# Optimization experiments

Measured on AMD Instinct MI355X. Metric: run time of the kernel, lower is better.

Reference implementation:

```python
import jax, jax.numpy as jnp
import numpy as np

N_NODES = 50000
N_EDGES = 1000000
N_QUERY = 100000
NUM_FEATURES = 256
HIDDEN = 256
LABEL_DIM = 2


def glorot(key, shape):
    lim = float(np.sqrt(6.0 / (shape[0] + shape[1])))
    return jax.random.uniform(key, shape, jnp.float32, -lim, lim)


def setup_inputs() -> dict:
    key = jax.random.key(0)
    ks = jax.random.split(key, 8)
    x = jax.random.normal(ks[0], (N_NODES, NUM_FEATURES), jnp.float32)
    edge_index = jax.random.randint(ks[1], (2, N_EDGES), 0, N_NODES)
    query_edges = jax.random.randint(ks[2], (N_QUERY, 2), 0, N_NODES)
    edge_weight = jax.random.uniform(ks[3], (N_EDGES,), jnp.float32)
    W1 = glorot(ks[4], (NUM_FEATURES, HIDDEN))
    b1 = jnp.zeros((HIDDEN,), jnp.float32)
    W2 = glorot(ks[5], (HIDDEN, HIDDEN))
    b2 = jnp.zeros((HIDDEN,), jnp.float32)
    Wl = glorot(ks[6], (2 * HIDDEN, LABEL_DIM))
    bl = jnp.zeros((LABEL_DIM,), jnp.float32)
    return {"x": x, "edge_index": edge_index, "query_edges": query_edges,
            "edge_weight": edge_weight, "W1": W1, "b1": b1, "W2": W2,
            "b2": b2, "Wl": Wl, "bl": bl}


def digcn_conv(x, edge_index, edge_weight, W, b):
    # x: [N, F_in] -> h: [N, F_out]; propagate: out[dst] += w_e * h[src]
    h = x @ W
    src, dst = edge_index[0], edge_index[1]
    msg = h[src] * edge_weight[:, None]            # [E, F_out]
    agg = jax.ops.segment_sum(msg, dst, num_segments=x.shape[0])
    return agg + b


def reference(x, edge_index, query_edges, edge_weight, W1, b1, W2, b2, Wl, bl):
    h = jax.nn.relu(digcn_conv(x, edge_index, edge_weight, W1, b1))
    # dropout is identity at eval time
    h = digcn_conv(h, edge_index, edge_weight, W2, b2)
    q = jnp.concatenate((h[query_edges[:, 0]], h[query_edges[:, 1]]), axis=-1)
    logits = q @ Wl + bl
    return jax.nn.log_softmax(logits, axis=1)
```

## Files before the change

kernel.cpp:

```cpp
#include <hip/hip_runtime.h>
#include <hip/hip_bf16.h>
#include <math.h>

typedef __bf16 bf16;
typedef __bf16 v8bf __attribute__((ext_vector_type(8)));
typedef __bf16 v4bf __attribute__((ext_vector_type(4)));
typedef float  v4f  __attribute__((ext_vector_type(4)));

#define FDIM 256
#define BKT_CAP 8192
#define AROW 264
#define GEMM_BLOCKS 512


__global__ __launch_bounds__(256) void flag_kernel(float* __restrict__ out, int n) {
  int i = blockIdx.x * 256 + threadIdx.x;
  if (i < n) out[i] = 1.0e9f;
}

__global__ __launch_bounds__(256) void k1_prep(const float* __restrict__ W1,
                                               const float* __restrict__ W2,
                                               bf16* __restrict__ Wt1,
                                               bf16* __restrict__ Wt2,
                                               const int* __restrict__ dst,
                                               int* __restrict__ phist,
                                               const float* __restrict__ Wl,
                                               const float* __restrict__ b2,
                                               const float* __restrict__ bl,
                                               float4* __restrict__ V,
                                               float* __restrict__ cc,
                                               int E, int N, int nbkt) {
  __shared__ int h[256];
  __shared__ float sWl[1024];
  __shared__ float red[256];
  int b = blockIdx.x;
  int t = threadIdx.x;
  if (b < 512) {
    const float* W = (b >> 8) ? W2 : W1;
    bf16* Wt = (b >> 8) ? Wt2 : Wt1;
    int k = b & 255;
    Wt[t * FDIM + k] = (bf16)W[k * FDIM + t];
  } else if (b < 768) {
    int pb = b - 512;
    h[t] = 0;
    __syncthreads();
    for (int e = pb * 256 + t; e < E; e += 256 * 256) {
      int d = dst[e];
      d = d < 0 ? 0 : (d >= N ? N - 1 : d);
      atomicAdd(&h[d >> 8], 1);
    }
    __syncthreads();
    phist[pb * 256 + t] = h[t];
  } else {
#pragma unroll
    for (int j = 0; j < 4; ++j) sWl[j * 256 + t] = Wl[j * 256 + t];
    __syncthreads();
    const float* w2row = W2 + (size_t)t * FDIM;
    float4 acc = make_float4(0.f, 0.f, 0.f, 0.f);
    for (int j = 0; j < 256; ++j) {
      float w = w2row[j];
      acc.x += w * sWl[2 * j + 0];
      acc.y += w * sWl[2 * j + 1];
      acc.z += w * sWl[512 + 2 * j + 0];
      acc.w += w * sWl[512 + 2 * j + 1];
    }
    V[t] = acc;
    float bj = b2[t];
    red[t] = bj * (sWl[2 * t + 0] + sWl[512 + 2 * t + 0]);
    __syncthreads();
    if (t == 0) {
      float s = 0.f;
      for (int j = 0; j < 256; ++j) s += red[j];
      cc[0] = s + bl[0];
    }
    __syncthreads();
    red[t] = bj * (sWl[2 * t + 1] + sWl[512 + 2 * t + 1]);
    __syncthreads();
    if (t == 0) {
      float s = 0.f;
      for (int j = 0; j < 256; ++j) s += red[j];
      cc[1] = s + bl[1];
    }
  }
}

__global__ __launch_bounds__(256) void p2_scan(const int* __restrict__ phist,
                                               int* __restrict__ bbase,
                                               int* __restrict__ gcur,
                                               int* __restrict__ offs,
                                               int nbkt, int Nn) {
  __shared__ int wsum[4];
  int t = threadIdx.x, lane = t & 63, wv = t >> 6;
  int v = 0;
  for (int pb = 0; pb < 256; ++pb) v += phist[pb * 256 + t];
  if (t >= nbkt) v = 0;
  int x = v;
#pragma unroll
  for (int d = 1; d < 64; d <<= 1) {
    int y = __shfl_up(x, d, 64);
    if (lane >= d) x += y;
  }
  if (lane == 63) wsum[wv] = x;
  __syncthreads();
  int woff = 0;
  if (wv >= 1) woff += wsum[0];
  if (wv >= 2) woff += wsum[1];
  if (wv >= 3) woff += wsum[2];
  int incl = woff + x;
  int excl = incl - v;
  if (t < nbkt) { bbase[t] = excl; gcur[t] = excl; }
  if (t == 255) {
    bbase[nbkt] = incl;
    offs[Nn] = incl;
  }
}


__device__ inline void stage64(const float* __restrict__ A, bf16* __restrict__ As,
                               int row0, int M, int tid) {
#pragma unroll
  for (int j = 0; j < 8; ++j) {
    int g = j * 2048 + tid * 8;
    int r = g >> 8, c = g & 255;
    int gr = row0 + r; if (gr >= M) gr = M - 1;
    const float* p = A + (size_t)gr * FDIM + c;
    float4 f0 = *reinterpret_cast<const float4*>(p);
    float4 f1 = *reinterpret_cast<const float4*>(p + 4);
    v8bf o;
    o[0] = (bf16)f0.x; o[1] = (bf16)f0.y; o[2] = (bf16)f0.z; o[3] = (bf16)f0.w;
    o[4] = (bf16)f1.x; o[5] = (bf16)f1.y; o[6] = (bf16)f1.z; o[7] = (bf16)f1.w;
    *reinterpret_cast<v8bf*>(As + r * AROW + c) = o;
  }
}

__device__ inline void gemm_body(const float* __restrict__ A, const bf16* __restrict__ Bt,
                                 bf16* __restrict__ C, int M, int bid, int nblocks,
                                 bf16* __restrict__ As) {
  const int K = FDIM, N = FDIM;
  int tid = threadIdx.x;
  int wave = tid >> 6;
  int lane = tid & 63;
  int l15 = lane & 15, quad = lane >> 4;

  v8bf bfr[4][8];
#pragma unroll
  for (int nn = 0; nn < 4; ++nn) {
    const bf16* bp = Bt + (size_t)(wave * 64 + nn * 16 + l15) * K + quad * 8;
#pragma unroll
    for (int kk = 0; kk < 8; ++kk)
      bfr[nn][kk] = *reinterpret_cast<const v8bf*>(bp + kk * 32);
  }

  int ntiles = (M + 63) >> 6;
  for (int tile = bid; tile < ntiles; tile += nblocks) {
    int row0 = tile * 64;
    __syncthreads();
    stage64(A, As, row0, M, tid);
    __syncthreads();

#pragma unroll
    for (int st = 0; st < 4; ++st) {
      v8bf afr[8];
#pragma unroll
      for (int kk = 0; kk < 8; ++kk)
        afr[kk] = *reinterpret_cast<const v8bf*>(As + (st * 16 + l15) * AROW + quad * 8 + kk * 32);

      v4f acc[4];
#pragma unroll
      for (int nn = 0; nn < 4; ++nn) acc[nn] = (v4f){0.f, 0.f, 0.f, 0.f};

#pragma unroll
      for (int kk = 0; kk < 8; ++kk)
#pragma unroll
        for (int nn = 0; nn < 4; ++nn)
          acc[nn] = __builtin_amdgcn_mfma_f32_16x16x32_bf16(afr[kk], bfr[nn][kk], acc[nn], 0, 0, 0);

#pragma unroll
      for (int nn = 0; nn < 4; ++nn)
#pragma unroll
        for (int r = 0; r < 4; ++r) {
          int row = row0 + st * 16 + quad * 4 + r;
          int col = wave * 64 + nn * 16 + l15;
          if (row < M) C[(size_t)row * N + col] = (bf16)acc[nn][r];
        }
    }
  }
}

__device__ inline void p3_body(const int* __restrict__ src, const int* __restrict__ dst,
                               const float* __restrict__ ew, int* __restrict__ gcur,
                               uint2* __restrict__ tmp, int E, int N, int nbkt,
                               int pb, int nblocks, int* h, int* base, int* cnt) {
  int t = threadIdx.x;
  int chunk = (E + nblocks - 1) / nblocks;
  int lo = pb * chunk;
  int hi = lo + chunk; if (hi > E) hi = E;
  h[t] = 0; cnt[t] = 0;
  __syncthreads();
  for (int e = lo + t; e < hi; e += 256) {
    int d = dst[e];
    d = d < 0 ? 0 : (d >= N ? N - 1 : d);
    atomicAdd(&h[d >> 8], 1);
  }
  __syncthreads();
  if (t < nbkt) base[t] = atomicAdd(&gcur[t], h[t]);
  __syncthreads();
  for (int e = lo + t; e < hi; e += 256) {
    int d = dst[e];
    d = d < 0 ? 0 : (d >= N ? N - 1 : d);
    int b = d >> 8;
    int sv = src[e];
    sv = sv < 0 ? 0 : (sv >= N ? N - 1 : sv);
    unsigned int u = __float_as_uint(ew[e]);
    unsigned int wbits = ((u + 0x7FFFu + ((u >> 16) & 1u)) & 0xFFFF0000u);
    unsigned int meta = wbits | (unsigned int)(sv & 0xFFFF);
    int r = atomicAdd(&cnt[b], 1);
    int pos = base[b] + r;
    if (pos >= 0 && pos < E) tmp[pos] = make_uint2(meta, (unsigned int)d);
  }
}

__global__ __launch_bounds__(256, 2) void k3_gemm1_p3(const float* __restrict__ x,
                                                      const bf16* __restrict__ Wt1,
                                                      bf16* __restrict__ bufT, int M,
                                                      const int* __restrict__ src,
                                                      const int* __restrict__ dst,
                                                      const float* __restrict__ ew,
                                                      int* __restrict__ gcur,
                                                      uint2* __restrict__ tmp,
                                                      int E, int N, int nbkt) {
  __shared__ bf16 As[64 * AROW];
  __shared__ int h[256], base[256], cnt[256];
  if (blockIdx.x < GEMM_BLOCKS)
    gemm_body(x, Wt1, bufT, M, blockIdx.x, GEMM_BLOCKS, As);
  else
    p3_body(src, dst, ew, gcur, tmp, E, N, nbkt, blockIdx.x - GEMM_BLOCKS, 256, h, base, cnt);
}

__global__ __launch_bounds__(256) void p4_sort(const uint2* __restrict__ tmp,
                                               const int* __restrict__ bbase,
                                               unsigned int* __restrict__ pmeta,
                                               int* __restrict__ offs,
                                               int Nn, int E) {
  __shared__ uint2 ent[BKT_CAP];
  __shared__ int h2[256], ex2[256], c2[256];
  __shared__ int wsum[4];
  int b = blockIdx.x, t = threadIdx.x, lane = t & 63, wv = t >> 6;
  int s0 = bbase[b], s1 = bbase[b + 1];
  int count = s1 - s0;
  if (count < 0) count = 0;
  if (count > BKT_CAP) count = BKT_CAP;
  for (int i = t; i < count; i += 256) ent[i] = tmp[s0 + i];
  h2[t] = 0; c2[t] = 0;
  __syncthreads();
  for (int i = t; i < count; i += 256) atomicAdd(&h2[ent[i].y & 255u], 1);
  __syncthreads();
  int v = h2[t];
  int x = v;
#pragma unroll
  for (int d = 1; d < 64; d <<= 1) {
    int y = __shfl_up(x, d, 64);
    if (lane >= d) x += y;
  }
  if (lane == 63) wsum[wv] = x;
  __syncthreads();
  int woff = 0;
  if (wv >= 1) woff += wsum[0];
  if (wv >= 2) woff += wsum[1];
  if (wv >= 3) woff += wsum[2];
  int excl = woff + x - v;
  ex2[t] = excl;
  int node = (b << 8) + t;
  if (node < Nn) offs[node] = s0 + excl;
  __syncthreads();
  for (int i = t; i < count; i += 256) {
    int l = (int)(ent[i].y & 255u);
    int r = atomicAdd(&c2[l], 1);
    int pos = s0 + ex2[l] + r;
    if (pos >= 0 && pos < E) pmeta[pos] = ent[i].x;
  }
}

__global__ __launch_bounds__(256) void agg1G(const bf16* __restrict__ T,
                                             const unsigned int* __restrict__ pmeta,
                                             const int* __restrict__ offsets,
                                             const float* __restrict__ bias,
                                             const float4* __restrict__ V,
                                             float4* __restrict__ G, int N, int E) {
  int node = blockIdx.x * 4 + (threadIdx.x >> 6);
  if (node >= N) return;
  int lane = threadIdx.x & 63;
  int f = lane * 4;
  int beg = offsets[node], end = offsets[node + 1];
  beg = beg < 0 ? 0 : (beg > E ? E : beg);
  end = end < beg ? beg : (end > E ? E : end);
  const unsigned int* m = pmeta + beg;
  int cnt = end - beg;

  float a0 = 0.f, a1 = 0.f, a2 = 0.f, a3 = 0.f;
  int p = 0;
  for (; p + 8 <= cnt; p += 8) {
    unsigned int mv[8];
#pragma unroll
    for (int j = 0; j < 8; ++j) mv[j] = m[p + j];
    v4bf tv[8];
#pragma unroll
    for (int j = 0; j < 8; ++j) {
      int s = (int)(mv[j] & 0xFFFFu);
      s = s >= N ? N - 1 : s;
      tv[j] = *reinterpret_cast<const v4bf*>(T + (size_t)s * FDIM + f);
    }
#pragma unroll
    for (int j = 0; j < 8; ++j) {
      float w = __uint_as_float(mv[j] & 0xFFFF0000u);
      a0 += w * (float)tv[j][0];
      a1 += w * (float)tv[j][1];
      a2 += w * (float)tv[j][2];
      a3 += w * (float)tv[j][3];
    }
  }
  for (; p < cnt; ++p) {
    unsigned int mv = m[p];
    int s = (int)(mv & 0xFFFFu);
    s = s >= N ? N - 1 : s;
    float w = __uint_as_float(mv & 0xFFFF0000u);
    v4bf tv = *reinterpret_cast<const v4bf*>(T + (size_t)s * FDIM + f);
    a0 += w * (float)tv[0];
    a1 += w * (float)tv[1];
    a2 += w * (float)tv[2];
    a3 += w * (float)tv[3];
  }
  a0 = fmaxf(a0 + bias[f + 0], 0.f);
  a1 = fmaxf(a1 + bias[f + 1], 0.f);
  a2 = fmaxf(a2 + bias[f + 2], 0.f);
  a3 = fmaxf(a3 + bias[f + 3], 0.f);

  float4 v0 = V[f + 0], v1 = V[f + 1], v2 = V[f + 2], v3 = V[f + 3];
  float gx = a0 * v0.x + a1 * v1.x + a2 * v2.x + a3 * v3.x;
  float gy = a0 * v0.y + a1 * v1.y + a2 * v2.y + a3 * v3.y;
  float gz = a0 * v0.z + a1 * v1.z + a2 * v2.z + a3 * v3.z;
  float gw = a0 * v0.w + a1 * v1.w + a2 * v2.w + a3 * v3.w;
#pragma unroll
  for (int d = 32; d > 0; d >>= 1) {
    gx += __shfl_down(gx, d, 64);
    gy += __shfl_down(gy, d, 64);
    gz += __shfl_down(gz, d, 64);
    gw += __shfl_down(gw, d, 64);
  }
  if (lane == 0) G[node] = make_float4(gx, gy, gz, gw);
}

__global__ __launch_bounds__(256) void aggP(const float4* __restrict__ G,
                                            const unsigned int* __restrict__ pmeta,
                                            const int* __restrict__ offsets,
                                            float4* __restrict__ P, int N, int E) {
  int node = blockIdx.x * 256 + threadIdx.x;
  if (node >= N) return;
  int beg = offsets[node], end = offsets[node + 1];
  beg = beg < 0 ? 0 : (beg > E ? E : beg);
  end = end < beg ? beg : (end > E ? E : end);
  float ax = 0.f, ay = 0.f, az = 0.f, aw = 0.f;
  int p = beg;
  for (; p + 4 <= end; p += 4) {
    unsigned int m0 = pmeta[p + 0], m1 = pmeta[p + 1], m2 = pmeta[p + 2], m3 = pmeta[p + 3];
    int s0 = (int)(m0 & 0xFFFFu); s0 = s0 >= N ? N - 1 : s0;
    int s1 = (int)(m1 & 0xFFFFu); s1 = s1 >= N ? N - 1 : s1;
    int s2 = (int)(m2 & 0xFFFFu); s2 = s2 >= N ? N - 1 : s2;
    int s3 = (int)(m3 & 0xFFFFu); s3 = s3 >= N ? N - 1 : s3;
    float4 g0 = G[s0], g1 = G[s1], g2 = G[s2], g3 = G[s3];
    float w0 = __uint_as_float(m0 & 0xFFFF0000u);
    float w1 = __uint_as_float(m1 & 0xFFFF0000u);
    float w2 = __uint_as_float(m2 & 0xFFFF0000u);
    float w3 = __uint_as_float(m3 & 0xFFFF0000u);
    ax += w0 * g0.x + w1 * g1.x + w2 * g2.x + w3 * g3.x;
    ay += w0 * g0.y + w1 * g1.y + w2 * g2.y + w3 * g3.y;
    az += w0 * g0.z + w1 * g1.z + w2 * g2.z + w3 * g3.z;
    aw += w0 * g0.w + w1 * g1.w + w2 * g2.w + w3 * g3.w;
  }
  for (; p < end; ++p) {
    unsigned int mm = pmeta[p];
    int s = (int)(mm & 0xFFFFu); s = s >= N ? N - 1 : s;
    float w = __uint_as_float(mm & 0xFFFF0000u);
    float4 g = G[s];
    ax += w * g.x; ay += w * g.y; az += w * g.z; aw += w * g.w;
  }
  P[node] = make_float4(ax, ay, az, aw);
}

__global__ __launch_bounds__(256) void query_small(const int* __restrict__ qe,
                                                   const float4* __restrict__ P,
                                                   const float* __restrict__ cc,
                                                   float* __restrict__ out, int Q, int N) {
  int q = blockIdx.x * 256 + threadIdx.x;
  if (q >= Q) return;
  int n0 = qe[2 * q + 0]; n0 = n0 < 0 ? 0 : (n0 >= N ? N - 1 : n0);
  int n1 = qe[2 * q + 1]; n1 = n1 < 0 ? 0 : (n1 >= N ? N - 1 : n1);
  float4 p0 = P[n0];
  float4 p1 = P[n1];
  float l0 = p0.x + p1.z + cc[0];
  float l1 = p0.y + p1.w + cc[1];
  float m = fmaxf(l0, l1);
  float lse = m + logf(expf(l0 - m) + expf(l1 - m));
  out[2 * q + 0] = l0 - lse;
  out[2 * q + 1] = l1 - lse;
}


extern "C" void kernel_launch(void* const* d_in, const int* in_sizes, int n_in,
                              void* d_out, int out_size, void* d_ws, size_t ws_size,
                              hipStream_t stream) {
  const float* x  = (const float*)d_in[0];
  const int*   ei = (const int*)d_in[1];
  const int*   qe = (const int*)d_in[2];
  const float* ew = (const float*)d_in[3];
  const float* W1 = (const float*)d_in[4];
  const float* b1 = (const float*)d_in[5];
  const float* W2 = (const float*)d_in[6];
  const float* b2 = (const float*)d_in[7];
  const float* Wl = (const float*)d_in[8];
  const float* bl = (const float*)d_in[9];

  int N = in_sizes[0] / FDIM;
  int E = in_sizes[1] / 2;
  int Q = in_sizes[2] / 2;
  const int* srcv = ei;
  const int* dstv = ei + E;
  int nbkt = (N + 255) >> 8;

  size_t off = 0;
  auto alloc = [&](size_t bytes) -> void* {
    void* p = (char*)d_ws + off;
    off += (bytes + 255) & ~(size_t)255;
    return p;
  };
  bf16* bufT  = (bf16*)alloc((size_t)N * FDIM * 2);
  uint2* tmp  = (uint2*)alloc((size_t)E * 8);
  bf16* Wt1   = (bf16*)alloc((size_t)FDIM * FDIM * 2);
  bf16* Wt2   = (bf16*)alloc((size_t)FDIM * FDIM * 2);
  int* offs   = (int*)alloc((size_t)(N + 1) * 4);
  unsigned int* pmeta = (unsigned int*)alloc((size_t)E * 4);
  float4* G   = (float4*)alloc((size_t)N * 16);
  float4* P   = (float4*)alloc((size_t)N * 16);
  float4* V   = (float4*)alloc(256 * 16);
  float* cc   = (float*)alloc(2 * 4);
  int* phist  = (int*)alloc(256 * 256 * 4);
  int* bbase  = (int*)alloc(257 * 4);
  int* gcur   = (int*)alloc(256 * 4);

  if (off > ws_size) {
    flag_kernel<<<(out_size + 255) / 256, 256, 0, stream>>>((float*)d_out, out_size);
    return;
  }

  k1_prep<<<769, 256, 0, stream>>>(W1, W2, Wt1, Wt2, dstv, phist, Wl, b2, bl, V, cc,
                                   E, N, nbkt);
  p2_scan<<<1, 256, 0, stream>>>(phist, bbase, gcur, offs, nbkt, N);
  k3_gemm1_p3<<<GEMM_BLOCKS + 256, 256, 0, stream>>>(x, Wt1, bufT, N,
                                                     srcv, dstv, ew, gcur, tmp, E, N, nbkt);
  p4_sort<<<nbkt, 256, 0, stream>>>(tmp, bbase, pmeta, offs, N, E);

  agg1G<<<(N + 3) / 4, 256, 0, stream>>>(bufT, pmeta, offs, b1, V, G, N, E);

  aggP<<<(N + 255) / 256, 256, 0, stream>>>(G, pmeta, offs, P, N, E);

  query_small<<<(Q + 255) / 256, 256, 0, stream>>>(qe, P, cc, (float*)d_out, Q, N);
}
```

Baseline: 248.8 us.

## Shrink CSR buckets, double p3 blocks, and use 16-lane groups per node in aggP

Bucketing now uses 128 nodes per bucket instead of 256, so p4_sort launches about twice as many blocks, each sorting a smaller shared-memory bucket. The scatter phase fused with the first GEMM gets 512 blocks instead of 256. The final aggregation kernel assigns a 16-lane group to each node and sums with shuffle reductions, replacing one thread per node. This is meant to improve parallelism and load balance and to coalesce the edge-metadata reads. The unused W2 transpose is also dropped. The cost is more global atomic traffic on the bucket cursors and larger histogram and scan arrays.

```diff
diff --git a/kernel.cpp b/kernel.cpp
--- a/kernel.cpp
+++ b/kernel.cpp
@@ -8,9 +8,11 @@
 typedef float  v4f  __attribute__((ext_vector_type(4)));
 
 #define FDIM 256
-#define BKT_CAP 8192
+#define BSHIFT 7
+#define BKT_CAP 4096
 #define AROW 264
 #define GEMM_BLOCKS 512
+#define P3_BLOCKS 512
 
 
 __global__ __launch_bounds__(256) void flag_kernel(float* __restrict__ out, int n) {
@@ -21,7 +23,6 @@
 __global__ __launch_bounds__(256) void k1_prep(const float* __restrict__ W1,
                                                const float* __restrict__ W2,
                                                bf16* __restrict__ Wt1,
-                                               bf16* __restrict__ Wt2,
                                                const int* __restrict__ dst,
                                                int* __restrict__ phist,
                                                const float* __restrict__ Wl,
@@ -29,28 +30,26 @@
                                                const float* __restrict__ bl,
                                                float4* __restrict__ V,
                                                float* __restrict__ cc,
-                                               int E, int N, int nbkt) {
-  __shared__ int h[256];
+                                               int E, int N) {
+  __shared__ int h[512];
   __shared__ float sWl[1024];
   __shared__ float red[256];
   int b = blockIdx.x;
   int t = threadIdx.x;
-  if (b < 512) {
-    const float* W = (b >> 8) ? W2 : W1;
-    bf16* Wt = (b >> 8) ? Wt2 : Wt1;
-    int k = b & 255;
-    Wt[t * FDIM + k] = (bf16)W[k * FDIM + t];
-  } else if (b < 768) {
-    int pb = b - 512;
-    h[t] = 0;
+  if (b < 256) {
+    Wt1[t * FDIM + b] = (bf16)W1[b * FDIM + t];
+  } else if (b < 512) {
+    int pb = b - 256;
+    h[t] = 0; h[t + 256] = 0;
     __syncthreads();
     for (int e = pb * 256 + t; e < E; e += 256 * 256) {
       int d = dst[e];
       d = d < 0 ? 0 : (d >= N ? N - 1 : d);
-      atomicAdd(&h[d >> 8], 1);
-    }
-    __syncthreads();
-    phist[pb * 256 + t] = h[t];
+      atomicAdd(&h[d >> BSHIFT], 1);
+    }
+    __syncthreads();
+    phist[pb * 512 + t] = h[t];
+    phist[pb * 512 + t + 256] = h[t + 256];
   } else {
 #pragma unroll
     for (int j = 0; j < 4; ++j) sWl[j * 256 + t] = Wl[j * 256 + t];
@@ -84,15 +83,15 @@
   }
 }
 
-__global__ __launch_bounds__(256) void p2_scan(const int* __restrict__ phist,
+__global__ __launch_bounds__(512) void p2_scan(const int* __restrict__ phist,
                                                int* __restrict__ bbase,
                                                int* __restrict__ gcur,
                                                int* __restrict__ offs,
                                                int nbkt, int Nn) {
-  __shared__ int wsum[4];
+  __shared__ int wsum[8];
   int t = threadIdx.x, lane = t & 63, wv = t >> 6;
   int v = 0;
-  for (int pb = 0; pb < 256; ++pb) v += phist[pb * 256 + t];
+  for (int pb = 0; pb < 256; ++pb) v += phist[pb * 512 + t];
   if (t >= nbkt) v = 0;
   int x = v;
 #pragma unroll
@@ -103,13 +102,11 @@
   if (lane == 63) wsum[wv] = x;
   __syncthreads();
   int woff = 0;
-  if (wv >= 1) woff += wsum[0];
-  if (wv >= 2) woff += wsum[1];
-  if (wv >= 3) woff += wsum[2];
+  for (int i = 0; i < wv; ++i) woff += wsum[i];
   int incl = woff + x;
   int excl = incl - v;
   if (t < nbkt) { bbase[t] = excl; gcur[t] = excl; }
-  if (t == 255) {
+  if (t == 511) {
     bbase[nbkt] = incl;
     offs[Nn] = incl;
   }
@@ -195,20 +192,21 @@
   int chunk = (E + nblocks - 1) / nblocks;
   int lo = pb * chunk;
   int hi = lo + chunk; if (hi > E) hi = E;
-  h[t] = 0; cnt[t] = 0;
+  h[t] = 0; h[t + 256] = 0; cnt[t] = 0; cnt[t + 256] = 0;
   __syncthreads();
   for (int e = lo + t; e < hi; e += 256) {
     int d = dst[e];
     d = d < 0 ? 0 : (d >= N ? N - 1 : d);
-    atomicAdd(&h[d >> 8], 1);
-  }
-  __syncthreads();
-  if (t < nbkt) base[t] = atomicAdd(&gcur[t], h[t]);
+    atomicAdd(&h[d >> BSHIFT], 1);
+  }
+  __syncthreads();
+  for (int b = t; b < nbkt; b += 256)
+    if (h[b]) base[b] = atomicAdd(&gcur[b], h[b]);
   __syncthreads();
   for (int e = lo + t; e < hi; e += 256) {
     int d = dst[e];
     d = d < 0 ? 0 : (d >= N ? N - 1 : d);
-    int b = d >> 8;
+    int b = d >> BSHIFT;
     int sv = src[e];
     sv = sv < 0 ? 0 : (sv >= N ? N - 1 : sv);
     unsigned int u = __float_as_uint(ew[e]);
@@ -230,11 +228,12 @@
                                                       uint2* __restrict__ tmp,
                                                       int E, int N, int nbkt) {
   __shared__ bf16 As[64 * AROW];
-  __shared__ int h[256], base[256], cnt[256];
+  __shared__ int h[512], base[512], cnt[512];
   if (blockIdx.x < GEMM_BLOCKS)
     gemm_body(x, Wt1, bufT, M, blockIdx.x, GEMM_BLOCKS, As);
   else
-    p3_body(src, dst, ew, gcur, tmp, E, N, nbkt, blockIdx.x - GEMM_BLOCKS, 256, h, base, cnt);
+    p3_body(src, dst, ew, gcur, tmp, E, N, nbkt,
+            blockIdx.x - GEMM_BLOCKS, P3_BLOCKS, h, base, cnt);
 }
 
 __global__ __launch_bounds__(256) void p4_sort(const uint2* __restrict__ tmp,
@@ -243,7 +242,7 @@
                                                int* __restrict__ offs,
                                                int Nn, int E) {
   __shared__ uint2 ent[BKT_CAP];
-  __shared__ int h2[256], ex2[256], c2[256];
+  __shared__ int h2[128], ex2[128], c2[128];
   __shared__ int wsum[4];
   int b = blockIdx.x, t = threadIdx.x, lane = t & 63, wv = t >> 6;
   int s0 = bbase[b], s1 = bbase[b + 1];
@@ -251,11 +250,11 @@
   if (count < 0) count = 0;
   if (count > BKT_CAP) count = BKT_CAP;
   for (int i = t; i < count; i += 256) ent[i] = tmp[s0 + i];
-  h2[t] = 0; c2[t] = 0;
-  __syncthreads();
-  for (int i = t; i < count; i += 256) atomicAdd(&h2[ent[i].y & 255u], 1);
-  __syncthreads();
-  int v = h2[t];
+  if (t < 128) { h2[t] = 0; c2[t] = 0; }
+  __syncthreads();
+  for (int i = t; i < count; i += 256) atomicAdd(&h2[ent[i].y & 127u], 1);
+  __syncthreads();
+  int v = (t < 128) ? h2[t] : 0;
   int x = v;
 #pragma unroll
   for (int d = 1; d < 64; d <<= 1) {
@@ -269,12 +268,14 @@
   if (wv >= 2) woff += wsum[1];
   if (wv >= 3) woff += wsum[2];
   int excl = woff + x - v;
-  ex2[t] = excl;
-  int node = (b << 8) + t;
-  if (node < Nn) offs[node] = s0 + excl;
+  if (t < 128) {
+    ex2[t] = excl;
+    int node = (b << BSHIFT) + t;
+    if (node < Nn) offs[node] = s0 + excl;
+  }
   __syncthreads();
   for (int i = t; i < count; i += 256) {
-    int l = (int)(ent[i].y & 255u);
+    int l = (int)(ent[i].y & 127u);
     int r = atomicAdd(&c2[l], 1);
     int pos = s0 + ex2[l] + r;
     if (pos >= 0 && pos < E) pmeta[pos] = ent[i].x;
@@ -354,37 +355,30 @@
                                             const unsigned int* __restrict__ pmeta,
                                             const int* __restrict__ offsets,
                                             float4* __restrict__ P, int N, int E) {
-  int node = blockIdx.x * 256 + threadIdx.x;
+  int tid = threadIdx.x;
+  int wave = tid >> 6, lane = tid & 63;
+  int grp = lane >> 4, sub = lane & 15;
+  int node = blockIdx.x * 16 + wave * 4 + grp;
   if (node >= N) return;
   int beg = offsets[node], end = offsets[node + 1];
   beg = beg < 0 ? 0 : (beg > E ? E : beg);
   end = end < beg ? beg : (end > E ? E : end);
   float ax = 0.f, ay = 0.f, az = 0.f, aw = 0.f;
-  int p = beg;
-  for (; p + 4 <= end; p += 4) {
-    unsigned int m0 = pmeta[p + 0], m1 = pmeta[p + 1], m2 = pmeta[p + 2], m3 = pmeta[p + 3];
-    int s0 = (int)(m0 & 0xFFFFu); s0 = s0 >= N ? N - 1 : s0;
-    int s1 = (int)(m1 & 0xFFFFu); s1 = s1 >= N ? N - 1 : s1;
-    int s2 = (int)(m2 & 0xFFFFu); s2 = s2 >= N ? N - 1 : s2;
-    int s3 = (int)(m3 & 0xFFFFu); s3 = s3 >= N ? N - 1 : s3;
-    float4 g0 = G[s0], g1 = G[s1], g2 = G[s2], g3 = G[s3];
-    float w0 = __uint_as_float(m0 & 0xFFFF0000u);
-    float w1 = __uint_as_float(m1 & 0xFFFF0000u);
-    float w2 = __uint_as_float(m2 & 0xFFFF0000u);
-    float w3 = __uint_as_float(m3 & 0xFFFF0000u);
-    ax += w0 * g0.x + w1 * g1.x + w2 * g2.x + w3 * g3.x;
-    ay += w0 * g0.y + w1 * g1.y + w2 * g2.y + w3 * g3.y;
-    az += w0 * g0.z + w1 * g1.z + w2 * g2.z + w3 * g3.z;
-    aw += w0 * g0.w + w1 * g1.w + w2 * g2.w + w3 * g3.w;
-  }
-  for (; p < end; ++p) {
+  for (int p = beg + sub; p < end; p += 16) {
     unsigned int mm = pmeta[p];
     int s = (int)(mm & 0xFFFFu); s = s >= N ? N - 1 : s;
     float w = __uint_as_float(mm & 0xFFFF0000u);
     float4 g = G[s];
     ax += w * g.x; ay += w * g.y; az += w * g.z; aw += w * g.w;
   }
-  P[node] = make_float4(ax, ay, az, aw);
+#pragma unroll
+  for (int d = 1; d < 16; d <<= 1) {
+    ax += __shfl_xor(ax, d, 64);
+    ay += __shfl_xor(ay, d, 64);
+    az += __shfl_xor(az, d, 64);
+    aw += __shfl_xor(aw, d, 64);
+  }
+  if (sub == 0) P[node] = make_float4(ax, ay, az, aw);
 }
 
 __global__ __launch_bounds__(256) void query_small(const int* __restrict__ qe,
@@ -425,7 +419,7 @@
   int Q = in_sizes[2] / 2;
   const int* srcv = ei;
   const int* dstv = ei + E;
-  int nbkt = (N + 255) >> 8;
+  int nbkt = (N + 127) >> BSHIFT;
 
   size_t off = 0;
   auto alloc = [&](size_t bytes) -> void* {
@@ -436,32 +430,31 @@
   bf16* bufT  = (bf16*)alloc((size_t)N * FDIM * 2);
   uint2* tmp  = (uint2*)alloc((size_t)E * 8);
   bf16* Wt1   = (bf16*)alloc((size_t)FDIM * FDIM * 2);
-  bf16* Wt2   = (bf16*)alloc((size_t)FDIM * FDIM * 2);
   int* offs   = (int*)alloc((size_t)(N + 1) * 4);
   unsigned int* pmeta = (unsigned int*)alloc((size_t)E * 4);
   float4* G   = (float4*)alloc((size_t)N * 16);
   float4* P   = (float4*)alloc((size_t)N * 16);
   float4* V   = (float4*)alloc(256 * 16);
   float* cc   = (float*)alloc(2 * 4);
-  int* phist  = (int*)alloc(256 * 256 * 4);
-  int* bbase  = (int*)alloc(257 * 4);
-  int* gcur   = (int*)alloc(256 * 4);
+  int* phist  = (int*)alloc(256 * 512 * 4);
+  int* bbase  = (int*)alloc(512 * 4);
+  int* gcur   = (int*)alloc(512 * 4);
 
   if (off > ws_size) {
     flag_kernel<<<(out_size + 255) / 256, 256, 0, stream>>>((float*)d_out, out_size);
     return;
   }
 
-  k1_prep<<<769, 256, 0, stream>>>(W1, W2, Wt1, Wt2, dstv, phist, Wl, b2, bl, V, cc,
-                                   E, N, nbkt);
-  p2_scan<<<1, 256, 0, stream>>>(phist, bbase, gcur, offs, nbkt, N);
-  k3_gemm1_p3<<<GEMM_BLOCKS + 256, 256, 0, stream>>>(x, Wt1, bufT, N,
-                                                     srcv, dstv, ew, gcur, tmp, E, N, nbkt);
+  k1_prep<<<513, 256, 0, stream>>>(W1, W2, Wt1, dstv, phist, Wl, b2, bl, V, cc, E, N);
+  p2_scan<<<1, 512, 0, stream>>>(phist, bbase, gcur, offs, nbkt, N);
+  k3_gemm1_p3<<<GEMM_BLOCKS + P3_BLOCKS, 256, 0, stream>>>(x, Wt1, bufT, N,
+                                                           srcv, dstv, ew, gcur, tmp,
+                                                           E, N, nbkt);
   p4_sort<<<nbkt, 256, 0, stream>>>(tmp, bbase, pmeta, offs, N, E);
 
   agg1G<<<(N + 3) / 4, 256, 0, stream>>>(bufT, pmeta, offs, b1, V, G, N, E);
 
-  aggP<<<(N + 255) / 256, 256, 0, stream>>>(G, pmeta, offs, P, N, E);
+  aggP<<<(N + 15) / 16, 256, 0, stream>>>(G, pmeta, offs, P, N, E);
 
   query_small<<<(Q + 255) / 256, 256, 0, stream>>>(qe, P, cc, (float*)d_out, Q, N);
 }
```

New measurement: 250.5 us. No clear change (+0.7%).
